# Optimization experiments

Hardware: AMD Instinct MI355X
Metric: run time of the kernel (lower is better)

The kernel has to match this reference:

```python
import jax, jax.numpy as jnp
import numpy as np

NUM_CLASSES = 20
NUM_BOXES = 2
INPUT_SIZE = 448.0
CONF_THR = 0.25
IOU_THR = 0.45
S = 7
EPS = 1e-6


def setup_inputs() -> dict:
    key = jax.random.key(0)
    x = jax.random.normal(key, (1, S, S, NUM_BOXES * 5 + NUM_CLASSES), dtype=jnp.float32)
    return {"x": x}


def _decode(x):
    # x: (1, S, S, nb*5 + nc) raw logits
    B, H, W, _ = x.shape
    p = jax.nn.sigmoid(x)
    # per-box confidences: (B, H, W, nb)
    conf = jnp.stack([p[..., NUM_CLASSES + 5 * i] for i in range(NUM_BOXES)], axis=-1)
    best = jnp.argmax(conf, axis=-1)                       # (B, H, W)
    oh = jax.nn.one_hot(best, NUM_BOXES, dtype=p.dtype)    # (B, H, W, nb)
    # select box coords / conf of the best box per cell
    pbox = sum(oh[..., i:i + 1] * p[..., NUM_CLASSES + 1 + 5 * i:NUM_CLASSES + 5 + 5 * i]
               for i in range(NUM_BOXES))                  # (B, H, W, 4) [cx, cy, w, h]
    pconf = jnp.sum(oh * conf, axis=-1, keepdims=True)     # (B, H, W, 1)
    gx = jnp.arange(W, dtype=p.dtype)
    gy = jnp.arange(H, dtype=p.dtype)
    grid = jnp.stack(jnp.meshgrid(gx, gy), axis=-1)        # (H, W, 2) -> [x, y]
    xy = pbox[..., 0:2] + grid                             # add cell offsets
    wh = pbox[..., 2:4] * jnp.asarray([W, H], dtype=p.dtype)
    stride = jnp.asarray([INPUT_SIZE / W, INPUT_SIZE / H] * 2, dtype=p.dtype)
    box = jnp.concatenate([xy, wh], axis=-1) * stride      # input-size scale
    pcls = jnp.argmax(p[..., :NUM_CLASSES], axis=-1, keepdims=True).astype(p.dtype)
    out = jnp.concatenate([pcls, pconf, box], axis=-1)     # (B, H, W, 6)
    return out.reshape(-1, H * W, 6)


def _iou_cxcywh(box, boxes):
    # box: (4,), boxes: (N, 4), both [cx, cy, w, h]
    b1_min = box[0:2] - box[2:4] / 2.0
    b1_max = box[0:2] + box[2:4] / 2.0
    b2_min = boxes[:, 0:2] - boxes[:, 2:4] / 2.0
    b2_max = boxes[:, 0:2] + boxes[:, 2:4] / 2.0
    inter_min = jnp.maximum(b1_min, b2_min)
    inter_max = jnp.minimum(b1_max, b2_max)
    inter_wh = jnp.clip(inter_max - inter_min, 0.0)
    inter = inter_wh[:, 0] * inter_wh[:, 1]
    a1 = jnp.abs((b1_max[0] - b1_min[0]) * (b1_max[1] - b1_min[1]))
    a2 = jnp.abs((b2_max[:, 0] - b2_min[:, 0]) * (b2_max[:, 1] - b2_min[:, 1]))
    return inter / (a1 + a2 - inter + EPS)


def _nms(boxes):
    # boxes: (N, 6) [cls, conf, cx, cy, w, h]
    # Greedy per-class NMS, jit-safe: fixed-size output, keep mask instead of
    # variable-length filtering. Equivalent to the source's while-loop NMS.
    N = boxes.shape[0]
    order = jnp.argsort(-boxes[:, 1])
    b = boxes[order]
    cls = b[:, 0]
    keep0 = b[:, 1] > CONF_THR  # conf threshold filter
    idx = jnp.arange(N)

    def body(i, keep):
        bi = b[i]
        ious = _iou_cxcywh(bi[2:6], b[:, 2:6])
        suppress = (idx > i) & keep[i] & (cls == bi[0]) & (ious >= IOU_THR)
        return keep & ~suppress

    keep = jax.lax.fori_loop(0, N, body, keep0)
    return b * keep[:, None].astype(b.dtype), keep


def reference(x):
    decoded = _decode(x)            # (1, 49, 6)
    boxes, keep = _nms(decoded[0])  # (49, 6) conf-sorted, zeroed where suppressed
    return boxes, keep
```

## Files before the change

kernel.cpp:

```cpp
#include <hip/hip_runtime.h>
#include <math.h>


#define NUM_CLASSES 20
#define S 7
#define NCELL 49
#define CONF_THR 0.25f
#define IOU_THR 0.45f
#define EPS_IOU 1e-6f
#define CELL_STRIDE 64.0f

__device__ __forceinline__ float sigmoidf(float v) {
    return 1.0f / (1.0f + expf(-v));
}

__global__ __launch_bounds__(64) void yolo_decode_nms(const float* __restrict__ x,
                                                      float* __restrict__ out) {
    const int j = threadIdx.x;

    __shared__ float s_box[NCELL][6];
    __shared__ float s_sorted[NCELL][6];

    if (j < NCELL) {
        const float* c = x + j * (NUM_CLASSES + 10);

        int ci = 0;
        float cmax = c[0];
        #pragma unroll
        for (int k = 1; k < NUM_CLASSES; ++k) {
            float v = c[k];
            if (v > cmax) { cmax = v; ci = k; }
        }

        float c0 = c[NUM_CLASSES + 0];
        float c1 = c[NUM_CLASSES + 5];
        int best = (c1 > c0) ? 1 : 0;
        int boff = NUM_CLASSES + 1 + 5 * best;

        float conf = sigmoidf(best ? c1 : c0);
        float bx = sigmoidf(c[boff + 0]);
        float by = sigmoidf(c[boff + 1]);
        float bw = sigmoidf(c[boff + 2]);
        float bh = sigmoidf(c[boff + 3]);

        int row = j / S, col = j % S;

        s_box[j][0] = (float)ci;
        s_box[j][1] = conf;
        s_box[j][2] = (bx + (float)col) * CELL_STRIDE;
        s_box[j][3] = (by + (float)row) * CELL_STRIDE;
        s_box[j][4] = bw * (float)S * CELL_STRIDE;
        s_box[j][5] = bh * (float)S * CELL_STRIDE;
    }
    __syncthreads();

    if (j < NCELL) {
        float myconf = s_box[j][1];
        int rank = 0;
        for (int k = 0; k < NCELL; ++k) {
            float ck = s_box[k][1];
            rank += (ck > myconf) || (ck == myconf && k < j);
        }
        #pragma unroll
        for (int t = 0; t < 6; ++t) s_sorted[rank][t] = s_box[j][t];
    }
    __syncthreads();

    float cls = 0.f, conf = 0.f, cx = 0.f, cy = 0.f, w = 0.f, h = 0.f;
    if (j < NCELL) {
        cls  = s_sorted[j][0];
        conf = s_sorted[j][1];
        cx   = s_sorted[j][2];
        cy   = s_sorted[j][3];
        w    = s_sorted[j][4];
        h    = s_sorted[j][5];
    }
    int keep = (j < NCELL) && (conf > CONF_THR);

    float minx = cx - 0.5f * w, maxx = cx + 0.5f * w;
    float miny = cy - 0.5f * h, maxy = cy + 0.5f * h;
    float area = fabsf(w * h);

    for (int i = 0; i < NCELL; ++i) {
        int   keep_i = __shfl(keep, i);
        float icls   = __shfl(cls,  i);
        float iminx  = __shfl(minx, i);
        float imaxx  = __shfl(maxx, i);
        float iminy  = __shfl(miny, i);
        float imaxy  = __shfl(maxy, i);
        float iarea  = __shfl(area, i);

        if (j > i && keep && keep_i && cls == icls) {
            float ix0 = fmaxf(minx, iminx);
            float iy0 = fmaxf(miny, iminy);
            float ix1 = fminf(maxx, imaxx);
            float iy1 = fminf(maxy, imaxy);
            float iw = fmaxf(ix1 - ix0, 0.0f);
            float ih = fmaxf(iy1 - iy0, 0.0f);
            float inter = iw * ih;
            float iou = inter / (iarea + area - inter + EPS_IOU);
            if (iou >= IOU_THR) keep = 0;
        }
    }

    if (j < NCELL) {
        float kf = keep ? 1.0f : 0.0f;
        out[j * 6 + 0] = cls  * kf;
        out[j * 6 + 1] = conf * kf;
        out[j * 6 + 2] = cx   * kf;
        out[j * 6 + 3] = cy   * kf;
        out[j * 6 + 4] = w    * kf;
        out[j * 6 + 5] = h    * kf;
        out[NCELL * 6 + j] = kf;
    }
}

extern "C" void kernel_launch(void* const* d_in, const int* in_sizes, int n_in,
                              void* d_out, int out_size, void* d_ws, size_t ws_size,
                              hipStream_t stream) {
    const float* x = (const float*)d_in[0];
    float* out = (float*)d_out;
    yolo_decode_nms<<<1, 64, 0, stream>>>(x, out);
}
```

Before: 61.99 us.

## Stage input into LDS with float4 loads and store precomputed box corners

The whole 1470-float input is copied into shared memory with coalesced float4 loads before decoding, replacing strided per-thread global reads. The sort now writes box corners and area instead of cx/cy/w/h. The NMS loop reads the pivot box from LDS broadcast rather than through several cross-lane shuffles. The output reconstructs cx/cy/w/h from the corners, which can introduce small floating-point rounding differences.

```diff
diff --git a/kernel.cpp b/kernel.cpp
--- a/kernel.cpp
+++ b/kernel.cpp
@@ -5,6 +5,7 @@
 #define NUM_CLASSES 20
 #define S 7
 #define NCELL 49
+#define NIN 1470
 #define CONF_THR 0.25f
 #define IOU_THR 0.45f
 #define EPS_IOU 1e-6f
@@ -18,11 +19,23 @@
                                                       float* __restrict__ out) {
     const int j = threadIdx.x;
 
-    __shared__ float s_box[NCELL][6];
-    __shared__ float s_sorted[NCELL][6];
+    __shared__ float s_in[1472];
+    __shared__ float s_sorted[NCELL][8];
+    __shared__ float s_conf[NCELL];
 
+    #pragma unroll
+    for (int t = 0; t < 6; ++t) {
+        int i4 = t * 64 + j;
+        if (i4 < NIN / 4) {
+            ((float4*)s_in)[i4] = ((const float4*)x)[i4];
+        }
+    }
+    if (j < 2) s_in[1468 + j] = x[1468 + j];
+    __syncthreads();
+
+    float cls = 0.f, conf = 0.f, cx = 0.f, cy = 0.f, w = 0.f, h = 0.f;
     if (j < NCELL) {
-        const float* c = x + j * (NUM_CLASSES + 10);
+        const float* c = s_in + j * (NUM_CLASSES + 10);
 
         int ci = 0;
         float cmax = c[0];
@@ -37,60 +50,64 @@
         int best = (c1 > c0) ? 1 : 0;
         int boff = NUM_CLASSES + 1 + 5 * best;
 
-        float conf = sigmoidf(best ? c1 : c0);
+        conf = sigmoidf(best ? c1 : c0);
         float bx = sigmoidf(c[boff + 0]);
         float by = sigmoidf(c[boff + 1]);
         float bw = sigmoidf(c[boff + 2]);
         float bh = sigmoidf(c[boff + 3]);
 
         int row = j / S, col = j % S;
+        cls = (float)ci;
+        cx = (bx + (float)col) * CELL_STRIDE;
+        cy = (by + (float)row) * CELL_STRIDE;
+        w  = bw * (float)S * CELL_STRIDE;
+        h  = bh * (float)S * CELL_STRIDE;
 
-        s_box[j][0] = (float)ci;
-        s_box[j][1] = conf;
-        s_box[j][2] = (bx + (float)col) * CELL_STRIDE;
-        s_box[j][3] = (by + (float)row) * CELL_STRIDE;
-        s_box[j][4] = bw * (float)S * CELL_STRIDE;
-        s_box[j][5] = bh * (float)S * CELL_STRIDE;
+        s_conf[j] = conf;
     }
     __syncthreads();
 
     if (j < NCELL) {
-        float myconf = s_box[j][1];
         int rank = 0;
         for (int k = 0; k < NCELL; ++k) {
-            float ck = s_box[k][1];
-            rank += (ck > myconf) || (ck == myconf && k < j);
+            float ck = s_conf[k];
+            rank += (ck > conf) || (ck == conf && k < j);
         }
-        #pragma unroll
-        for (int t = 0; t < 6; ++t) s_sorted[rank][t] = s_box[j][t];
+        float minx = cx - 0.5f * w, maxx = cx + 0.5f * w;
+        float miny = cy - 0.5f * h, maxy = cy + 0.5f * h;
+        s_sorted[rank][0] = cls;
+        s_sorted[rank][1] = conf;
+        s_sorted[rank][2] = minx;
+        s_sorted[rank][3] = miny;
+        s_sorted[rank][4] = maxx;
+        s_sorted[rank][5] = maxy;
+        s_sorted[rank][6] = fabsf(w * h);
     }
     __syncthreads();
 
-    float cls = 0.f, conf = 0.f, cx = 0.f, cy = 0.f, w = 0.f, h = 0.f;
+    float mcls = 0.f, mconf = 0.f, minx = 0.f, miny = 0.f,
+          maxx = 0.f, maxy = 0.f, area = 0.f;
     if (j < NCELL) {
-        cls  = s_sorted[j][0];
-        conf = s_sorted[j][1];
-        cx   = s_sorted[j][2];
-        cy   = s_sorted[j][3];
-        w    = s_sorted[j][4];
-        h    = s_sorted[j][5];
+        mcls  = s_sorted[j][0];
+        mconf = s_sorted[j][1];
+        minx  = s_sorted[j][2];
+        miny  = s_sorted[j][3];
+        maxx  = s_sorted[j][4];
+        maxy  = s_sorted[j][5];
+        area  = s_sorted[j][6];
     }
-    int keep = (j < NCELL) && (conf > CONF_THR);
-
-    float minx = cx - 0.5f * w, maxx = cx + 0.5f * w;
-    float miny = cy - 0.5f * h, maxy = cy + 0.5f * h;
-    float area = fabsf(w * h);
+    int keep = (j < NCELL) && (mconf > CONF_THR);
 
     for (int i = 0; i < NCELL; ++i) {
-        int   keep_i = __shfl(keep, i);
-        float icls   = __shfl(cls,  i);
-        float iminx  = __shfl(minx, i);
-        float imaxx  = __shfl(maxx, i);
-        float iminy  = __shfl(miny, i);
-        float imaxy  = __shfl(maxy, i);
-        float iarea  = __shfl(area, i);
+        int keep_i = __shfl(keep, i);
+        float icls  = s_sorted[i][0];
+        float iminx = s_sorted[i][2];
+        float iminy = s_sorted[i][3];
+        float imaxx = s_sorted[i][4];
+        float imaxy = s_sorted[i][5];
+        float iarea = s_sorted[i][6];
 
-        if (j > i && keep && keep_i && cls == icls) {
+        if (j > i && keep && keep_i && mcls == icls) {
             float ix0 = fmaxf(minx, iminx);
             float iy0 = fmaxf(miny, iminy);
             float ix1 = fminf(maxx, imaxx);
@@ -105,12 +122,16 @@
 
     if (j < NCELL) {
         float kf = keep ? 1.0f : 0.0f;
-        out[j * 6 + 0] = cls  * kf;
-        out[j * 6 + 1] = conf * kf;
-        out[j * 6 + 2] = cx   * kf;
-        out[j * 6 + 3] = cy   * kf;
-        out[j * 6 + 4] = w    * kf;
-        out[j * 6 + 5] = h    * kf;
+        float ocx = 0.5f * (minx + maxx);
+        float ocy = 0.5f * (miny + maxy);
+        float ow  = maxx - minx;
+        float oh  = maxy - miny;
+        out[j * 6 + 0] = mcls  * kf;
+        out[j * 6 + 1] = mconf * kf;
+        out[j * 6 + 2] = ocx * kf;
+        out[j * 6 + 3] = ocy * kf;
+        out[j * 6 + 4] = ow  * kf;
+        out[j * 6 + 5] = oh  * kf;
         out[NCELL * 6 + j] = kf;
     }
 }
```

New measurement: 65.12 us. +5.0%, slower.
